# Kernel optimization log

Hardware: AMD Instinct MI355X
Metric: run time of the kernel (lower is better)

The kernel has to match this reference:

```python
import jax, jax.numpy as jnp
import numpy as np
import math


def wn_linear(x, v, g, b):
    # PyTorch weight_norm with dim=0: W[i] = g[i] * v[i] / ||v[i]||
    w = g[:, None] * v / jnp.linalg.norm(v, axis=1, keepdims=True)  # [out, in]
    return x @ w.T + b


def setup_inputs() -> dict:
    key = jax.random.key(0)
    ks = jax.random.split(key, 11)
    B, QC, KC, C, H, W = 8, 384, 384, 512, 32, 32
    s = 0.02
    return {
        "q": jax.random.normal(ks[0], (B, QC, H, W), jnp.float32),
        "k": jax.random.normal(ks[1], (B, KC, H, W), jnp.float32),
        "Wq_v": jax.random.normal(ks[2], (C, QC), jnp.float32) * s,
        "Wq_g": jax.random.uniform(ks[3], (C,), jnp.float32, 0.5, 1.5),
        "bq": jax.random.normal(ks[4], (C,), jnp.float32) * s,
        "Wk_v": jax.random.normal(ks[5], (C, KC), jnp.float32) * s,
        "Wk_g": jax.random.uniform(ks[6], (C,), jnp.float32, 0.5, 1.5),
        "bk": jax.random.normal(ks[7], (C,), jnp.float32) * s,
        "Wv_v": jax.random.normal(ks[8], (C, KC), jnp.float32) * s,
        "Wv_g": jax.random.uniform(ks[9], (C,), jnp.float32, 0.5, 1.5),
        "bv": jax.random.normal(ks[10], (C,), jnp.float32) * s,
    }


def reference(q, k, Wq_v, Wq_g, bq, Wk_v, Wk_g, bk, Wv_v, Wv_g, bv):
    NB_HEAD = 8
    B, _, H, W = k.shape
    S = H * W
    C = Wq_v.shape[0]
    D = C // NB_HEAD  # head_dim

    qf = q.reshape(B, q.shape[1], S).transpose(0, 2, 1)  # [B,S,QC]
    kf = k.reshape(B, k.shape[1], S).transpose(0, 2, 1)  # [B,S,KC]

    def heads(x):  # [B,S,C] -> [B,NH,S,D]
        return x.reshape(B, S, NB_HEAD, D).transpose(0, 2, 1, 3)

    qh = heads(wn_linear(qf, Wq_v, Wq_g, bq))
    kh = heads(wn_linear(kf, Wk_v, Wk_g, bk))
    vh = heads(wn_linear(kf, Wv_v, Wv_g, bv))

    attn = jnp.einsum("bhqd,bhkd->bhqk", qh, kh) / math.sqrt(D)
    # mask = triu(ones,1).t() -> strictly lower triangular allowed (no diagonal)
    allowed = jnp.tril(jnp.ones((S, S), bool), -1)
    attn = jnp.where(allowed, attn, jnp.float32(-10000.0))
    attn = jax.nn.softmax(attn, axis=-1)
    # start_mask zeroes row 0 of the attention weights (post-softmax multiply)
    start_mask = (jnp.arange(S) > 0).astype(attn.dtype)[None, None, :, None]
    attn = attn * start_mask
    # dropout in eval mode -> identity

    out = jnp.einsum("bhqk,bhkd->bhqd", attn, vh)  # [B,NH,S,D]
    out = out.transpose(0, 2, 1, 3).reshape(B, H, W, C).transpose(0, 3, 1, 2)
    return out
```

## Files before the change

kernel.cpp:

```cpp
#include <hip/hip_runtime.h>
#include <hip/hip_bf16.h>

typedef __attribute__((ext_vector_type(8))) __bf16 bf16x8;
typedef __attribute__((ext_vector_type(4))) float f32x4;

__device__ __forceinline__ f32x4 mfma16(bf16x8 a, bf16x8 b, f32x4 c) {
    return __builtin_amdgcn_mfma_f32_16x16x32_bf16(a, b, c, 0, 0, 0);
}

__device__ __forceinline__ unsigned short f2bf(float x) {
    union { float f; unsigned int u; } cv; cv.f = x;
    unsigned int r = cv.u + 0x7FFFu + ((cv.u >> 16) & 1u);
    return (unsigned short)(r >> 16);
}

__device__ __forceinline__ unsigned pack2(float a, float b) {
    return (unsigned)f2bf(a) | ((unsigned)f2bf(b) << 16);
}

__device__ __forceinline__ unsigned pk2(float a, float b) {
    float2 f2; f2.x = a; f2.y = b;
    __hip_bfloat162 h = __float22bfloat162_rn(f2);
    return *(unsigned*)&h;
}

__device__ __forceinline__ float fast_exp2(float x) {
    float r;
    asm("v_exp_f32 %0, %1" : "=v"(r) : "v"(x));
    return r;
}

__device__ __forceinline__ void gload_lds16(const void* g, void* l) {
    __builtin_amdgcn_global_load_lds(
        (const __attribute__((address_space(1))) unsigned int*)g,
        (__attribute__((address_space(3))) unsigned int*)l, 16, 0, 0);
}

__global__ __launch_bounds__(256) void prep_kernel(
    const float* __restrict__ q, const float* __restrict__ k,
    const float* __restrict__ Wq_v, const float* __restrict__ Wq_g,
    const float* __restrict__ Wk_v, const float* __restrict__ Wk_g,
    const float* __restrict__ Wv_v, const float* __restrict__ Wv_g,
    unsigned short* __restrict__ qT, unsigned short* __restrict__ kT,
    unsigned short* __restrict__ Wn)
{
    __shared__ float tile[32][33];
    int z = blockIdx.z;
    int t = threadIdx.x;
    if (z == 16) {
        int w = t >> 6, lane = t & 63;
        int idx = (blockIdx.y * 32 + blockIdx.x) * 4 + w;
        int proj = idx >> 9, o = idx & 511;
        const float* v = (proj == 0 ? Wq_v : proj == 1 ? Wk_v : Wv_v) + (size_t)o * 384;
        const float* g = (proj == 0 ? Wq_g : proj == 1 ? Wk_g : Wv_g);
        float vals[6];
        float ss = 0.f;
#pragma unroll
        for (int i = 0; i < 6; ++i) { vals[i] = v[lane + i * 64]; ss += vals[i] * vals[i]; }
#pragma unroll
        for (int off = 1; off < 64; off <<= 1) ss += __shfl_xor(ss, off, 64);
        float scale = g[o] * rsqrtf(ss);
        unsigned short* dst = Wn + ((size_t)proj * 512 + o) * 384;
#pragma unroll
        for (int i = 0; i < 6; ++i) dst[lane + i * 64] = f2bf(vals[i] * scale);
        return;
    }
    int tx = t & 31, ty = t >> 5;
    const float* src = (z < 8 ? q : k) + (size_t)(z & 7) * 384 * 1024;
    unsigned short* dst = (z < 8 ? qT : kT) + (size_t)(z & 7) * 1024 * 384;
    int c0 = blockIdx.y * 32, s0 = blockIdx.x * 32;
#pragma unroll
    for (int j = 0; j < 4; ++j)
        tile[ty + j * 8][tx] = src[(size_t)(c0 + ty + j * 8) * 1024 + s0 + tx];
    __syncthreads();
#pragma unroll
    for (int j = 0; j < 4; ++j)
        dst[(size_t)(s0 + ty + j * 8) * 384 + c0 + tx] = f2bf(tile[tx][ty + j * 8]);
}

__global__ __launch_bounds__(256) void proj_gemm(
    const unsigned short* __restrict__ qT, const unsigned short* __restrict__ kT,
    const unsigned short* __restrict__ Wn,
    const float* __restrict__ bq, const float* __restrict__ bk, const float* __restrict__ bv,
    unsigned short* __restrict__ Qp, unsigned short* __restrict__ Kp,
    unsigned short* __restrict__ Vt)
{
    __shared__ __align__(16) unsigned short Asm[2][128 * 32];
    __shared__ __align__(16) unsigned short Bsm[2][128 * 32];
    int zb = blockIdx.z; int proj = zb >> 3, b = zb & 7;
    const unsigned short* A = (proj == 0 ? qT : kT) + (size_t)b * 1024 * 384;
    const unsigned short* Bw = Wn + (size_t)proj * 512 * 384;
    const float* bias = proj == 0 ? bq : (proj == 1 ? bk : bv);
    int m0 = blockIdx.x * 128, n0 = blockIdx.y * 128;
    int t = threadIdx.x, w = t >> 6, lane = t & 63;
    int fr = lane & 15, fq = lane >> 4;
    int wm = (w >> 1) * 64, wn = (w & 1) * 64;

    f32x4 acc[4][4];
#pragma unroll
    for (int i = 0; i < 4; ++i)
#pragma unroll
        for (int j = 0; j < 4; ++j) acc[i][j] = (f32x4){0.f, 0.f, 0.f, 0.f};

    const unsigned short* asrc = A + (size_t)(m0 + w * 16 + (lane >> 2)) * 384 + (lane & 3) * 8;
    const unsigned short* bsrc = Bw + (size_t)(n0 + w * 16 + (lane >> 2)) * 384 + (lane & 3) * 8;

    auto stageAB = [&](int k0, int bufi) {
        gload_lds16(asrc + k0, &Asm[bufi][w * 512]);
        gload_lds16(asrc + k0 + (size_t)64 * 384, &Asm[bufi][w * 512 + 2048]);
        gload_lds16(bsrc + k0, &Bsm[bufi][w * 512]);
        gload_lds16(bsrc + k0 + (size_t)64 * 384, &Bsm[bufi][w * 512 + 2048]);
    };

    stageAB(0, 0);
    for (int ks = 0; ks < 12; ++ks) {
        if (ks < 11) {
            stageAB((ks + 1) * 32, (ks + 1) & 1);
            asm volatile("s_waitcnt vmcnt(4)" ::: "memory");
        } else {
            asm volatile("s_waitcnt vmcnt(0)" ::: "memory");
        }
        __builtin_amdgcn_s_barrier();
        int bi = ks & 1;
        bf16x8 af[4], bfr[4];
#pragma unroll
        for (int i = 0; i < 4; ++i)
            af[i] = *(const bf16x8*)&Asm[bi][(wm + i * 16 + fr) * 32 + fq * 8];
#pragma unroll
        for (int i = 0; i < 4; ++i)
            bfr[i] = *(const bf16x8*)&Bsm[bi][(wn + i * 16 + fr) * 32 + fq * 8];
#pragma unroll
        for (int mi = 0; mi < 4; ++mi)
#pragma unroll
            for (int ni = 0; ni < 4; ++ni)
                acc[mi][ni] = mfma16(af[mi], bfr[ni], acc[mi][ni]);
        asm volatile("s_waitcnt lgkmcnt(0)" ::: "memory");
        __builtin_amdgcn_s_barrier();
    }

    if (proj == 2) {
#pragma unroll
        for (int mi = 0; mi < 4; ++mi)
#pragma unroll
            for (int ni = 0; ni < 4; ++ni) {
                int c = n0 + wn + ni * 16 + fr;
                int s0 = m0 + wm + mi * 16 + fq * 4;
                float bc = bias[c];
                unsigned lo = pack2(acc[mi][ni][0] + bc, acc[mi][ni][1] + bc);
                unsigned hi = pack2(acc[mi][ni][2] + bc, acc[mi][ni][3] + bc);
                uint2 u; u.x = lo; u.y = hi;
                *(uint2*)&Vt[(((size_t)b * 512 + c) * 1024 + s0)] = u;
            }
    } else {
        unsigned short* Out = (proj == 0 ? Qp : Kp) + (size_t)b * 1024 * 512;
#pragma unroll
        for (int mi = 0; mi < 4; ++mi)
#pragma unroll
            for (int ni = 0; ni < 4; ++ni)
#pragma unroll
                for (int r = 0; r < 4; ++r) {
                    int c = n0 + wn + ni * 16 + fr;
                    int s = m0 + wm + mi * 16 + fq * 4 + r;
                    Out[(size_t)s * 512 + c] = f2bf(acc[mi][ni][r] + bias[c]);
                }
    }
}

__global__ __launch_bounds__(256, 4) void attn_kernel(
    const unsigned short* __restrict__ Qp, const unsigned short* __restrict__ Kp,
    const unsigned short* __restrict__ Vt, float* __restrict__ out)
{
    __shared__ __align__(16) unsigned short Kl[2][64 * 64];
    __shared__ __align__(16) unsigned short Vl[2][64 * 64];
    __shared__ __align__(16) unsigned short Pl[4][16 * 64];
    const float SCL = 0.125f * 1.44269504089f;
    int pj = blockIdx.x;
    int bh = blockIdx.y, b = bh >> 3, h = bh & 7;
    int t = threadIdx.x, w = t >> 6, lane = t & 63;
    int fr = lane & 15, fq = lane >> 4;
    int sub = lane >> 3;
    int sw = 8 * ((lane & 7) ^ sub);
    int swz = 8 * (fr & 7);
    const unsigned short* Qb = Qp + ((size_t)b * 1024) * 512 + h * 64;
    const unsigned short* Kb = Kp + ((size_t)b * 1024) * 512 + h * 64;
    const unsigned short* VTb = Vt + ((size_t)b * 512 + h * 64) * 1024;

    auto stage = [&](int kt, int bufi) {
        int kbase = kt * 64;
        int c0 = (w & 1) * 4;
        if (w < 2) {
#pragma unroll
            for (int i = 0; i < 4; ++i) {
                int c = c0 + i;
                gload_lds16(Kb + (size_t)(kbase + c * 8 + sub) * 512 + sw,
                            &Kl[bufi][c * 512]);
            }
        } else {
#pragma unroll
            for (int i = 0; i < 4; ++i) {
                int c = c0 + i;
                gload_lds16(VTb + (size_t)(c * 8 + sub) * 1024 + kbase + sw,
                            &Vl[bufi][c * 512]);
            }
        }
    };

    int cur = 0;
#pragma unroll 1
    for (int ph = 0; ph < 2; ++ph) {
        int qtile = ph == 0 ? pj : 15 - pj;
        int row0 = qtile * 64 + w * 16;
        int nt = qtile + 1;

        bf16x8 qf0 = *(const bf16x8*)(Qb + (size_t)(row0 + fr) * 512 + fq * 8);
        bf16x8 qf1 = *(const bf16x8*)(Qb + (size_t)(row0 + fr) * 512 + 32 + fq * 8);

        f32x4 Ot[4];
#pragma unroll
        for (int f = 0; f < 4; ++f) Ot[f] = (f32x4){0.f, 0.f, 0.f, 0.f};
        float M = -128.f, L = 0.f;

        stage(0, cur);
        for (int kt = 0; kt < nt; ++kt) {
            int kbase = kt * 64;
            if (kt + 1 < nt) {
                stage(kt + 1, cur ^ 1);
                asm volatile("s_waitcnt vmcnt(4)" ::: "memory");
            } else {
                asm volatile("s_waitcnt vmcnt(0)" ::: "memory");
            }
            __builtin_amdgcn_s_barrier();

            f32x4 Sacc[4];
#pragma unroll
            for (int kg = 0; kg < 4; ++kg) Sacc[kg] = (f32x4){0.f, 0.f, 0.f, 0.f};
#pragma unroll
            for (int kg = 0; kg < 4; ++kg) {
                bf16x8 k0 = *(const bf16x8*)&Kl[cur][(kg * 16 + fr) * 64 + ((fq * 8) ^ swz)];
                bf16x8 k1 = *(const bf16x8*)&Kl[cur][(kg * 16 + fr) * 64 + ((32 + fq * 8) ^ swz)];
                Sacc[kg] = mfma16(k0, qf0, Sacc[kg]);
                Sacc[kg] = mfma16(k1, qf1, Sacc[kg]);
            }

            int qrow = row0 + fr;
            float e[4][4];
            float vmax = -3e38f;
#pragma unroll
            for (int kg = 0; kg < 4; ++kg)
#pragma unroll
                for (int r = 0; r < 4; ++r) {
                    int key = kbase + kg * 16 + fq * 4 + r;
                    float sv = (key < qrow) ? Sacc[kg][r] * SCL : -3e38f;
                    e[kg][r] = sv;
                    vmax = fmaxf(vmax, sv);
                }
            vmax = fmaxf(vmax, __shfl_xor(vmax, 16, 64));
            vmax = fmaxf(vmax, __shfl_xor(vmax, 32, 64));
            if (__any(vmax > M + 8.f)) {
                float Mn = fmaxf(M, vmax);
                float al = fast_exp2(M - Mn);
                L *= al;
                M = Mn;
#pragma unroll
                for (int f = 0; f < 4; ++f) {
                    Ot[f][0] *= al; Ot[f][1] *= al; Ot[f][2] *= al; Ot[f][3] *= al;
                }
            }
            float rs = 0.f;
#pragma unroll
            for (int kg = 0; kg < 4; ++kg)
#pragma unroll
                for (int r = 0; r < 4; ++r) {
                    float ee = fast_exp2(e[kg][r] - M);
                    e[kg][r] = ee;
                    rs += ee;
                }
            rs += __shfl_xor(rs, 16, 64);
            rs += __shfl_xor(rs, 32, 64);
            L += rs;

#pragma unroll
            for (int kg = 0; kg < 4; ++kg) {
                uint2 u;
                u.x = pk2(e[kg][0], e[kg][1]);
                u.y = pk2(e[kg][2], e[kg][3]);
                *(uint2*)&Pl[w][fr * 64 + ((kg * 16 + fq * 4) ^ swz)] = u;
            }
            bf16x8 pb0 = *(const bf16x8*)&Pl[w][fr * 64 + ((fq * 8) ^ swz)];
            bf16x8 pb1 = *(const bf16x8*)&Pl[w][fr * 64 + ((32 + fq * 8) ^ swz)];

#pragma unroll
            for (int f = 0; f < 4; ++f) {
                bf16x8 a0 = *(const bf16x8*)&Vl[cur][(f * 16 + fr) * 64 + ((fq * 8) ^ swz)];
                bf16x8 a1 = *(const bf16x8*)&Vl[cur][(f * 16 + fr) * 64 + ((32 + fq * 8) ^ swz)];
                Ot[f] = mfma16(a0, pb0, Ot[f]);
                Ot[f] = mfma16(a1, pb1, Ot[f]);
            }

            asm volatile("s_waitcnt lgkmcnt(0)" ::: "memory");
            __builtin_amdgcn_s_barrier();
            cur ^= 1;
        }

        float rcp = (L > 0.f) ? 1.f / L : 0.f;
        int q = row0 + fr;
#pragma unroll
        for (int f = 0; f < 4; ++f)
#pragma unroll
            for (int rr = 0; rr < 4; ++rr) {
                int d = f * 16 + fq * 4 + rr;
                out[((size_t)b * 512 + h * 64 + d) * 1024 + q] = Ot[f][rr] * rcp;
            }
    }
}

extern "C" void kernel_launch(void* const* d_in, const int* in_sizes, int n_in,
                              void* d_out, int out_size, void* d_ws, size_t ws_size,
                              hipStream_t stream) {
    const float* q    = (const float*)d_in[0];
    const float* k    = (const float*)d_in[1];
    const float* Wq_v = (const float*)d_in[2];
    const float* Wq_g = (const float*)d_in[3];
    const float* bq   = (const float*)d_in[4];
    const float* Wk_v = (const float*)d_in[5];
    const float* Wk_g = (const float*)d_in[6];
    const float* bk   = (const float*)d_in[7];
    const float* Wv_v = (const float*)d_in[8];
    const float* Wv_g = (const float*)d_in[9];
    const float* bv   = (const float*)d_in[10];
    float* out = (float*)d_out;

    char* ws = (char*)d_ws;
    unsigned short* qT = (unsigned short*)(ws + 0);
    unsigned short* kT = (unsigned short*)(ws + 6291456);
    unsigned short* Wn = (unsigned short*)(ws + 12582912);
    unsigned short* Qp = (unsigned short*)(ws + 13762560);
    unsigned short* Kp = (unsigned short*)(ws + 22151168);
    unsigned short* Vt = (unsigned short*)(ws + 30539776);

    prep_kernel<<<dim3(32, 12, 17), dim3(256), 0, stream>>>(
        q, k, Wq_v, Wq_g, Wk_v, Wk_g, Wv_v, Wv_g, qT, kT, Wn);
    proj_gemm<<<dim3(8, 4, 24), dim3(256), 0, stream>>>(qT, kT, Wn, bq, bk, bv, Qp, Kp, Vt);
    attn_kernel<<<dim3(8, 64), dim3(256), 0, stream>>>(Qp, Kp, Vt, out);
}
```

Before: 66.31 us.

## Give each attention wave 32 query rows and pack prep transpose stores

The attention kernel now runs 2 waves per block, each handling 32 query rows (two 16-row groups). Each K/V fragment read from LDS is reused for twice as many MFMAs, which cuts LDS traffic per unit of compute and raises per-wave ILP. The cost is higher register pressure, fewer waves per block to hide latency, and 8 outstanding loads per wave instead of 4. Separately, the prep transpose writes two bf16 values per 32-bit store instead of single 16-bit stores.

Measured after the change: 72.45 us. +9.3%, slower.

```diff
diff --git a/kernel.cpp b/kernel.cpp
--- a/kernel.cpp
+++ b/kernel.cpp
@@ -73,9 +73,13 @@
     for (int j = 0; j < 4; ++j)
         tile[ty + j * 8][tx] = src[(size_t)(c0 + ty + j * 8) * 1024 + s0 + tx];
     __syncthreads();
-#pragma unroll
-    for (int j = 0; j < 4; ++j)
-        dst[(size_t)(s0 + ty + j * 8) * 384 + c0 + tx] = f2bf(tile[tx][ty + j * 8]);
+    int cp = tx & 15;
+#pragma unroll
+    for (int j = 0; j < 2; ++j) {
+        int ss = ty + (tx >> 4) * 8 + j * 16;
+        *(unsigned*)&dst[(size_t)(s0 + ss) * 384 + c0 + 2 * cp] =
+            pk2(tile[2 * cp][ss], tile[2 * cp + 1][ss]);
+    }
 }
 
 __global__ __launch_bounds__(256) void proj_gemm(
@@ -166,13 +170,13 @@
     }
 }
 
-__global__ __launch_bounds__(256, 4) void attn_kernel(
+__global__ __launch_bounds__(128, 2) void attn_kernel(
     const unsigned short* __restrict__ Qp, const unsigned short* __restrict__ Kp,
     const unsigned short* __restrict__ Vt, float* __restrict__ out)
 {
     __shared__ __align__(16) unsigned short Kl[2][64 * 64];
     __shared__ __align__(16) unsigned short Vl[2][64 * 64];
-    __shared__ __align__(16) unsigned short Pl[4][16 * 64];
+    __shared__ __align__(16) unsigned short Pl[2][32 * 64];
     const float SCL = 0.125f * 1.44269504089f;
     int pj = blockIdx.x;
     int bh = blockIdx.y, b = bh >> 3, h = bh & 7;
@@ -187,21 +191,16 @@
 
     auto stage = [&](int kt, int bufi) {
         int kbase = kt * 64;
-        int c0 = (w & 1) * 4;
-        if (w < 2) {
-#pragma unroll
-            for (int i = 0; i < 4; ++i) {
-                int c = c0 + i;
-                gload_lds16(Kb + (size_t)(kbase + c * 8 + sub) * 512 + sw,
-                            &Kl[bufi][c * 512]);
-            }
+        if (w == 0) {
+#pragma unroll
+            for (int i = 0; i < 8; ++i)
+                gload_lds16(Kb + (size_t)(kbase + i * 8 + sub) * 512 + sw,
+                            &Kl[bufi][i * 512]);
         } else {
 #pragma unroll
-            for (int i = 0; i < 4; ++i) {
-                int c = c0 + i;
-                gload_lds16(VTb + (size_t)(c * 8 + sub) * 1024 + kbase + sw,
-                            &Vl[bufi][c * 512]);
-            }
+            for (int i = 0; i < 8; ++i)
+                gload_lds16(VTb + (size_t)(i * 8 + sub) * 1024 + kbase + sw,
+                            &Vl[bufi][i * 512]);
         }
     };
 
@@ -209,92 +208,103 @@
 #pragma unroll 1
     for (int ph = 0; ph < 2; ++ph) {
         int qtile = ph == 0 ? pj : 15 - pj;
-        int row0 = qtile * 64 + w * 16;
+        int row0 = qtile * 64 + w * 32;
         int nt = qtile + 1;
 
-        bf16x8 qf0 = *(const bf16x8*)(Qb + (size_t)(row0 + fr) * 512 + fq * 8);
-        bf16x8 qf1 = *(const bf16x8*)(Qb + (size_t)(row0 + fr) * 512 + 32 + fq * 8);
-
-        f32x4 Ot[4];
-#pragma unroll
-        for (int f = 0; f < 4; ++f) Ot[f] = (f32x4){0.f, 0.f, 0.f, 0.f};
-        float M = -128.f, L = 0.f;
+        bf16x8 qf[2][2];
+#pragma unroll
+        for (int qg = 0; qg < 2; ++qg)
+#pragma unroll
+            for (int sl = 0; sl < 2; ++sl)
+                qf[qg][sl] = *(const bf16x8*)(Qb + (size_t)(row0 + qg * 16 + fr) * 512 + sl * 32 + fq * 8);
+
+        f32x4 Ot[4][2];
+#pragma unroll
+        for (int f = 0; f < 4; ++f) { Ot[f][0] = (f32x4){0,0,0,0}; Ot[f][1] = (f32x4){0,0,0,0}; }
+        float M[2] = {-128.f, -128.f}, L[2] = {0.f, 0.f};
 
         stage(0, cur);
         for (int kt = 0; kt < nt; ++kt) {
             int kbase = kt * 64;
             if (kt + 1 < nt) {
                 stage(kt + 1, cur ^ 1);
-                asm volatile("s_waitcnt vmcnt(4)" ::: "memory");
+                asm volatile("s_waitcnt vmcnt(8)" ::: "memory");
             } else {
                 asm volatile("s_waitcnt vmcnt(0)" ::: "memory");
             }
             __builtin_amdgcn_s_barrier();
 
-            f32x4 Sacc[4];
-#pragma unroll
-            for (int kg = 0; kg < 4; ++kg) Sacc[kg] = (f32x4){0.f, 0.f, 0.f, 0.f};
+            f32x4 Sacc[2][4];
+#pragma unroll
+            for (int kg = 0; kg < 4; ++kg) { Sacc[0][kg] = (f32x4){0,0,0,0}; Sacc[1][kg] = (f32x4){0,0,0,0}; }
 #pragma unroll
             for (int kg = 0; kg < 4; ++kg) {
                 bf16x8 k0 = *(const bf16x8*)&Kl[cur][(kg * 16 + fr) * 64 + ((fq * 8) ^ swz)];
                 bf16x8 k1 = *(const bf16x8*)&Kl[cur][(kg * 16 + fr) * 64 + ((32 + fq * 8) ^ swz)];
-                Sacc[kg] = mfma16(k0, qf0, Sacc[kg]);
-                Sacc[kg] = mfma16(k1, qf1, Sacc[kg]);
-            }
-
-            int qrow = row0 + fr;
-            float e[4][4];
-            float vmax = -3e38f;
-#pragma unroll
-            for (int kg = 0; kg < 4; ++kg)
-#pragma unroll
-                for (int r = 0; r < 4; ++r) {
-                    int key = kbase + kg * 16 + fq * 4 + r;
-                    float sv = (key < qrow) ? Sacc[kg][r] * SCL : -3e38f;
-                    e[kg][r] = sv;
-                    vmax = fmaxf(vmax, sv);
+                Sacc[0][kg] = mfma16(k0, qf[0][0], Sacc[0][kg]);
+                Sacc[0][kg] = mfma16(k1, qf[0][1], Sacc[0][kg]);
+                Sacc[1][kg] = mfma16(k0, qf[1][0], Sacc[1][kg]);
+                Sacc[1][kg] = mfma16(k1, qf[1][1], Sacc[1][kg]);
+            }
+
+#pragma unroll
+            for (int qg = 0; qg < 2; ++qg) {
+                int qrow = row0 + qg * 16 + fr;
+                float vmax = -3e38f;
+#pragma unroll
+                for (int kg = 0; kg < 4; ++kg)
+#pragma unroll
+                    for (int r = 0; r < 4; ++r) {
+                        int key = kbase + kg * 16 + fq * 4 + r;
+                        float sv = (key < qrow) ? Sacc[qg][kg][r] * SCL : -3e38f;
+                        Sacc[qg][kg][r] = sv;
+                        vmax = fmaxf(vmax, sv);
+                    }
+                vmax = fmaxf(vmax, __shfl_xor(vmax, 16, 64));
+                vmax = fmaxf(vmax, __shfl_xor(vmax, 32, 64));
+                if (__any(vmax > M[qg] + 8.f)) {
+                    float Mn = fmaxf(M[qg], vmax);
+                    float al = fast_exp2(M[qg] - Mn);
+                    L[qg] *= al;
+                    M[qg] = Mn;
+#pragma unroll
+                    for (int f = 0; f < 4; ++f) {
+                        Ot[f][qg][0] *= al; Ot[f][qg][1] *= al;
+                        Ot[f][qg][2] *= al; Ot[f][qg][3] *= al;
+                    }
                 }
-            vmax = fmaxf(vmax, __shfl_xor(vmax, 16, 64));
-            vmax = fmaxf(vmax, __shfl_xor(vmax, 32, 64));
-            if (__any(vmax > M + 8.f)) {
-                float Mn = fmaxf(M, vmax);
-                float al = fast_exp2(M - Mn);
-                L *= al;
-                M = Mn;
-#pragma unroll
-                for (int f = 0; f < 4; ++f) {
-                    Ot[f][0] *= al; Ot[f][1] *= al; Ot[f][2] *= al; Ot[f][3] *= al;
+                float rs = 0.f;
+#pragma unroll
+                for (int kg = 0; kg < 4; ++kg) {
+                    float e0 = fast_exp2(Sacc[qg][kg][0] - M[qg]);
+                    float e1 = fast_exp2(Sacc[qg][kg][1] - M[qg]);
+                    float e2 = fast_exp2(Sacc[qg][kg][2] - M[qg]);
+                    float e3 = fast_exp2(Sacc[qg][kg][3] - M[qg]);
+                    rs += (e0 + e1) + (e2 + e3);
+                    uint2 u;
+                    u.x = pk2(e0, e1);
+                    u.y = pk2(e2, e3);
+                    *(uint2*)&Pl[w][(qg * 16 + fr) * 64 + ((kg * 16 + fq * 4) ^ swz)] = u;
                 }
-            }
-            float rs = 0.f;
-#pragma unroll
-            for (int kg = 0; kg < 4; ++kg)
-#pragma unroll
-                for (int r = 0; r < 4; ++r) {
-                    float ee = fast_exp2(e[kg][r] - M);
-                    e[kg][r] = ee;
-                    rs += ee;
-                }
-            rs += __shfl_xor(rs, 16, 64);
-            rs += __shfl_xor(rs, 32, 64);
-            L += rs;
-
-#pragma unroll
-            for (int kg = 0; kg < 4; ++kg) {
-                uint2 u;
-                u.x = pk2(e[kg][0], e[kg][1]);
-                u.y = pk2(e[kg][2], e[kg][3]);
-                *(uint2*)&Pl[w][fr * 64 + ((kg * 16 + fq * 4) ^ swz)] = u;
-            }
-            bf16x8 pb0 = *(const bf16x8*)&Pl[w][fr * 64 + ((fq * 8) ^ swz)];
-            bf16x8 pb1 = *(const bf16x8*)&Pl[w][fr * 64 + ((32 + fq * 8) ^ swz)];
-
+                rs += __shfl_xor(rs, 16, 64);
+                rs += __shfl_xor(rs, 32, 64);
+                L[qg] += rs;
+            }
+
+            bf16x8 pb[2][2];
+#pragma unroll
+            for (int qg = 0; qg < 2; ++qg)
+#pragma unroll
+                for (int sl = 0; sl < 2; ++sl)
+                    pb[qg][sl] = *(const bf16x8*)&Pl[w][(qg * 16 + fr) * 64 + ((sl * 32 + fq * 8) ^ swz)];
 #pragma unroll
             for (int f = 0; f < 4; ++f) {
                 bf16x8 a0 = *(const bf16x8*)&Vl[cur][(f * 16 + fr) * 64 + ((fq * 8) ^ swz)];
                 bf16x8 a1 = *(const bf16x8*)&Vl[cur][(f * 16 + fr) * 64 + ((32 + fq * 8) ^ swz)];
-                Ot[f] = mfma16(a0, pb0, Ot[f]);
-                Ot[f] = mfma16(a1, pb1, Ot[f]);
+                Ot[f][0] = mfma16(a0, pb[0][0], Ot[f][0]);
+                Ot[f][0] = mfma16(a1, pb[0][1], Ot[f][0]);
+                Ot[f][1] = mfma16(a0, pb[1][0], Ot[f][1]);
+                Ot[f][1] = mfma16(a1, pb[1][1], Ot[f][1]);
             }
 
             asm volatile("s_waitcnt lgkmcnt(0)" ::: "memory");
@@ -302,15 +312,18 @@
             cur ^= 1;
         }
 
-        float rcp = (L > 0.f) ? 1.f / L : 0.f;
-        int q = row0 + fr;
-#pragma unroll
-        for (int f = 0; f < 4; ++f)
-#pragma unroll
-            for (int rr = 0; rr < 4; ++rr) {
-                int d = f * 16 + fq * 4 + rr;
-                out[((size_t)b * 512 + h * 64 + d) * 1024 + q] = Ot[f][rr] * rcp;
-            }
+#pragma unroll
+        for (int qg = 0; qg < 2; ++qg) {
+            float rcp = (L[qg] > 0.f) ? 1.f / L[qg] : 0.f;
+            int q = row0 + qg * 16 + fr;
+#pragma unroll
+            for (int f = 0; f < 4; ++f)
+#pragma unroll
+                for (int rr = 0; rr < 4; ++rr) {
+                    int d = f * 16 + fq * 4 + rr;
+                    out[((size_t)b * 512 + h * 64 + d) * 1024 + q] = Ot[f][qg][rr] * rcp;
+                }
+        }
     }
 }
 
@@ -341,5 +354,5 @@
     prep_kernel<<<dim3(32, 12, 17), dim3(256), 0, stream>>>(
         q, k, Wq_v, Wq_g, Wk_v, Wk_g, Wv_v, Wv_g, qT, kT, Wn);
     proj_gemm<<<dim3(8, 4, 24), dim3(256), 0, stream>>>(qT, kT, Wn, bq, bk, bv, Qp, Kp, Vt);
-    attn_kernel<<<dim3(8, 64), dim3(256), 0, stream>>>(Qp, Kp, Vt, out);
-}
+    attn_kernel<<<dim3(8, 64), dim3(128), 0, stream>>>(Qp, Kp, Vt, out);
+}
```
